# Kernel tuning notes

Measured on AMD Instinct MI355X. Metric: run time of the kernel, lower is better.

The kernel has to match this reference:

```python
import jax, jax.numpy as jnp
import numpy as np

B, S, D, H = 4, 2048, 1024, 16
HD = D // H  # head_dim = 64


def setup_inputs() -> dict:
    key = jax.random.key(0)
    ks = jax.random.split(key, 11)
    scale = 1.0 / np.sqrt(D)
    q = jax.random.normal(ks[0], (B, S, D), jnp.float32)
    k = jax.random.normal(ks[1], (B, S, D), jnp.float32)
    v = jax.random.normal(ks[2], (B, S, D), jnp.float32)
    # causal mask, broadcastable over [B, H, Sq, Sk]
    mask = jnp.tril(jnp.ones((S, S), bool))[None, None, :, :]
    Wq = jax.random.normal(ks[3], (D, D), jnp.float32) * scale
    bq = jnp.zeros((D,), jnp.float32)
    Wk = jax.random.normal(ks[4], (D, D), jnp.float32) * scale
    bk = jnp.zeros((D,), jnp.float32)
    Wv = jax.random.normal(ks[5], (D, D), jnp.float32) * scale
    bv = jnp.zeros((D,), jnp.float32)
    Wo = jax.random.normal(ks[6], (D, D), jnp.float32) * scale
    bo = jnp.zeros((D,), jnp.float32)
    return {"q": q, "k": k, "v": v, "mask": mask,
            "Wq": Wq, "bq": bq, "Wk": Wk, "bk": bk,
            "Wv": Wv, "bv": bv, "Wo": Wo, "bo": bo}


def reference(q, k, v, mask, Wq, bq, Wk, bk, Wv, bv, Wo, bo):
    b, sq, _ = q.shape
    sk = k.shape[1]
    # projections (torch Linear: x @ W.T + b)
    qh = (q @ Wq.T + bq).reshape(b, sq, H, HD)
    kh = (k @ Wk.T + bk).reshape(b, sk, H, HD)
    vh = (v @ Wv.T + bv).reshape(b, sk, H, HD)
    # scaled dot-product attention: [b, h, sq, sk]
    scores = jnp.einsum('bqhd,bkhd->bhqk', qh, kh) / jnp.sqrt(jnp.float32(HD))
    scores = jnp.where(mask, scores, jnp.float32(-jnp.inf))
    attn = jax.nn.softmax(scores, axis=-1)
    out = jnp.einsum('bhqk,bkhd->bqhd', attn, vh).reshape(b, sq, D)
    return out @ Wo.T + bo
```

## Files before the change

kernel.cpp:

```cpp
#include <hip/hip_runtime.h>
#include <hip/hip_bf16.h>
#include <cstdint>
#include <cstddef>

typedef __attribute__((ext_vector_type(4))) float f32x4;
typedef __attribute__((ext_vector_type(8))) __bf16 bf16x8;

constexpr int Bc = 4, Sc = 2048, Dc = 1024, Hc = 16, HDc = 64;
constexpr int Mrows = Bc * Sc;
constexpr int Kdim = Dc;

__device__ __forceinline__ void gload_lds16(const void* g, void* lds) {
  __builtin_amdgcn_global_load_lds(
      (const __attribute__((address_space(1))) void*)g,
      (__attribute__((address_space(3))) void*)lds, 16, 0, 0);
}

__global__ void cvt4_f32_to_bf16(const float* __restrict__ s0, const float* __restrict__ s1,
                                 const float* __restrict__ s2, const float* __restrict__ s3,
                                 __bf16* __restrict__ d0, __bf16* __restrict__ d1,
                                 __bf16* __restrict__ d2, __bf16* __restrict__ d3, int n4each) {
  int i = blockIdx.x * blockDim.x + threadIdx.x;
  int which = i / n4each, j = i - which * n4each;
  const float* s = which == 0 ? s0 : which == 1 ? s1 : which == 2 ? s2 : s3;
  __bf16* d = which == 0 ? d0 : which == 1 ? d1 : which == 2 ? d2 : d3;
  float4 f = ((const float4*)s)[j];
  union { __bf16 h[4]; uint2 u; } p;
  p.h[0] = (__bf16)f.x; p.h[1] = (__bf16)f.y;
  p.h[2] = (__bf16)f.z; p.h[3] = (__bf16)f.w;
  ((uint2*)d)[j] = p.u;
}

__global__ __launch_bounds__(256, 2)
void gemm_qkv(const float* __restrict__ qin, const float* __restrict__ kin,
              const float* __restrict__ vin, const __bf16* __restrict__ Wcat,
              const float* __restrict__ bq, const float* __restrict__ bk,
              const float* __restrict__ bv,
              __bf16* __restrict__ Qh, __bf16* __restrict__ Kh,
              __bf16* __restrict__ Vt, float qscale)
{
  __shared__ __align__(16) __bf16 As[128 * 32];
  __shared__ __align__(16) __bf16 Bs[128 * 32];
  const int tid = threadIdx.x;
  const int wave = tid >> 6, lane = tid & 63;
  const int wr = wave >> 1, wc = wave & 1;
  const int r = lane & 15, hi = lane >> 4;
  const int lin = (int)blockIdx.y * 24 + (int)blockIdx.x;
  const int xcd = lin & 7, s8 = lin >> 3;
  const int my = (xcd << 3) | (s8 / 24);
  const int mx = s8 % 24;
  const int m0 = my * 128, n0 = mx * 128;
  const int proj = n0 >> 10;
  const float* Xa = proj == 0 ? qin : proj == 1 ? kin : vin;

  f32x4 acc[4][4] = {};

  for (int k0 = 0; k0 < Kdim; k0 += 32) {
    #pragma unroll
    for (int c = 0; c < 2; ++c) {
      int chunk = c * 256 + tid;
      int row = chunk >> 2;
      int cw = chunk & 3;
      int hc = cw ^ (row & 3);
      const float* src = Xa + (size_t)(m0 + row) * Kdim + k0 + hc * 8;
      float4 f0 = *(const float4*)src;
      float4 f1 = *(const float4*)(src + 4);
      union { __bf16 h[8]; uint4 u; } pk;
      pk.h[0] = (__bf16)f0.x; pk.h[1] = (__bf16)f0.y;
      pk.h[2] = (__bf16)f0.z; pk.h[3] = (__bf16)f0.w;
      pk.h[4] = (__bf16)f1.x; pk.h[5] = (__bf16)f1.y;
      pk.h[6] = (__bf16)f1.z; pk.h[7] = (__bf16)f1.w;
      *(uint4*)&As[(size_t)chunk * 8] = pk.u;
    }
    #pragma unroll
    for (int c = 0; c < 2; ++c) {
      int chunk = c * 256 + wave * 64 + lane;
      int row = chunk >> 2;
      int hc = (chunk & 3) ^ (row & 3);
      gload_lds16(Wcat + (size_t)(n0 + row) * Kdim + k0 + hc * 8,
                  &Bs[(size_t)(c * 256 + wave * 64) * 8]);
    }
    __syncthreads();
    bf16x8 af[4], bfr[4];
    #pragma unroll
    for (int m = 0; m < 4; ++m) {
      int rowl = wr * 64 + m * 16 + r;
      af[m] = *(const bf16x8*)&As[rowl * 32 + ((hi ^ (rowl & 3)) * 8)];
    }
    #pragma unroll
    for (int n = 0; n < 4; ++n) {
      int rowl = wc * 64 + n * 16 + r;
      bfr[n] = *(const bf16x8*)&Bs[rowl * 32 + ((hi ^ (rowl & 3)) * 8)];
    }
    #pragma unroll
    for (int m = 0; m < 4; ++m)
      #pragma unroll
      for (int n = 0; n < 4; ++n)
        acc[m][n] = __builtin_amdgcn_mfma_f32_16x16x32_bf16(af[m], bfr[n], acc[m][n], 0, 0, 0);
    __syncthreads();
  }

  const float* bias = proj == 0 ? bq : proj == 1 ? bk : bv;
  if (proj < 2) {
    __bf16* out = proj == 0 ? Qh : Kh;
    const float sc = proj == 0 ? qscale : 1.0f;
    #pragma unroll
    for (int m = 0; m < 4; ++m)
      #pragma unroll
      for (int n = 0; n < 4; ++n)
        #pragma unroll
        for (int rg = 0; rg < 4; ++rg) {
          int row_g = m0 + wr * 64 + m * 16 + hi * 4 + rg;
          int col_g = n0 + wc * 64 + n * 16 + r;
          int c = col_g & 1023, h = c >> 6, d = c & 63;
          int b = row_g >> 11, s = row_g & (Sc - 1);
          float v = (acc[m][n][rg] + bias[c]) * sc;
          out[((((size_t)b * Hc + h) * Sc + s) << 6) + d] = (__bf16)v;
        }
  } else {
    #pragma unroll
    for (int m = 0; m < 4; ++m)
      #pragma unroll
      for (int n = 0; n < 4; ++n) {
        int row0 = m0 + wr * 64 + m * 16 + hi * 4;
        int col_g = n0 + wc * 64 + n * 16 + r;
        int c = col_g & 1023, h = c >> 6, d = c & 63;
        int b = row0 >> 11, s = row0 & (Sc - 1);
        union { __bf16 hh[4]; uint2 u; } w;
        #pragma unroll
        for (int rg = 0; rg < 4; ++rg)
          w.hh[rg] = (__bf16)(acc[m][n][rg] + bias[c]);
        *(uint2*)&Vt[((((size_t)b * Hc + h) * HDc + d) << 11) + s] = w.u;
      }
  }
}

__global__ __launch_bounds__(256, 2)
void gemm_out(const __bf16* __restrict__ A, const __bf16* __restrict__ Bw,
              const float* __restrict__ bias, float* __restrict__ outp)
{
  __shared__ __align__(16) __bf16 As[128 * 32];
  __shared__ __align__(16) __bf16 Bs[128 * 32];
  const int tid = threadIdx.x;
  const int wave = tid >> 6, lane = tid & 63;
  const int wr = wave >> 1, wc = wave & 1;
  const int r = lane & 15, hi = lane >> 4;
  const int lin = (int)blockIdx.y * 8 + (int)blockIdx.x;
  const int xcd = lin & 7, s8 = lin >> 3;
  const int m0 = (((xcd << 3) | (s8 >> 3)) ) * 128;
  const int n0 = (s8 & 7) * 128;

  f32x4 acc[4][4] = {};

  for (int k0 = 0; k0 < Kdim; k0 += 32) {
    #pragma unroll
    for (int c = 0; c < 2; ++c) {
      int chunk = c * 256 + wave * 64 + lane;
      int row = chunk >> 2;
      int hc = (chunk & 3) ^ (row & 3);
      gload_lds16(A  + (size_t)(m0 + row) * Kdim + k0 + hc * 8,
                  &As[(size_t)(c * 256 + wave * 64) * 8]);
      gload_lds16(Bw + (size_t)(n0 + row) * Kdim + k0 + hc * 8,
                  &Bs[(size_t)(c * 256 + wave * 64) * 8]);
    }
    __syncthreads();
    bf16x8 af[4], bfr[4];
    #pragma unroll
    for (int m = 0; m < 4; ++m) {
      int rowl = wr * 64 + m * 16 + r;
      af[m] = *(const bf16x8*)&As[rowl * 32 + ((hi ^ (rowl & 3)) * 8)];
    }
    #pragma unroll
    for (int n = 0; n < 4; ++n) {
      int rowl = wc * 64 + n * 16 + r;
      bfr[n] = *(const bf16x8*)&Bs[rowl * 32 + ((hi ^ (rowl & 3)) * 8)];
    }
    #pragma unroll
    for (int m = 0; m < 4; ++m)
      #pragma unroll
      for (int n = 0; n < 4; ++n)
        acc[m][n] = __builtin_amdgcn_mfma_f32_16x16x32_bf16(af[m], bfr[n], acc[m][n], 0, 0, 0);
    __syncthreads();
  }

  #pragma unroll
  for (int m = 0; m < 4; ++m)
    #pragma unroll
    for (int n = 0; n < 4; ++n)
      #pragma unroll
      for (int rg = 0; rg < 4; ++rg) {
        int row_g = m0 + wr * 64 + m * 16 + hi * 4 + rg;
        int col_g = n0 + wc * 64 + n * 16 + r;
        outp[(size_t)row_g * Dc + col_g] = acc[m][n][rg] + bias[col_g];
      }
}

__global__ __launch_bounds__(128, 2)
void attn_causal(const __bf16* __restrict__ Qh, const __bf16* __restrict__ Kh,
                 const __bf16* __restrict__ Vt, __bf16* __restrict__ outp)
{
  const int tid = threadIdx.x;
  const int wave = tid >> 6, lane = tid & 63;
  const int r = lane & 15, hi = lane >> 4;
  const int lin = (int)blockIdx.y * 32 + (int)blockIdx.x;
  const int xcd = lin & 7, s8 = lin >> 3;
  const int bh = (xcd << 3) | (s8 >> 5);
  const int px = s8 & 31;
  const int qh = wave ? (63 - px) : px;
  const int q0 = qh * 32;
  const __bf16* Q = Qh + (size_t)bh * (Sc * HDc);
  const __bf16* K = Kh + (size_t)bh * (Sc * HDc);
  const __bf16* V = Vt + (size_t)bh * (HDc * Sc);

  bf16x8 qf[2][2];
  #pragma unroll
  for (int m = 0; m < 2; ++m)
    #pragma unroll
    for (int kc = 0; kc < 2; ++kc)
      qf[m][kc] = *(const bf16x8*)&Q[(size_t)(q0 + m * 16 + r) * 64 + kc * 32 + hi * 8];

  f32x4 o_acc[2][4] = {};
  float mrow[2], lrow[2];
  #pragma unroll
  for (int m = 0; m < 2; ++m) { mrow[m] = -1e30f; lrow[m] = 0.f; }

  const int T = (qh >> 1) + 1;
  const int qloc_base = (qh & 1) * 32;

  bf16x8 kf[4][2], vf[4][2], pb[2][2];

  #pragma unroll
  for (int n = 0; n < 4; ++n)
    #pragma unroll
    for (int kc = 0; kc < 2; ++kc) {
      kf[n][kc] = *(const bf16x8*)&K[(size_t)(n * 16 + r) * 64 + kc * 32 + hi * 8];
      vf[n][kc] = *(const bf16x8*)&V[(size_t)(n * 16 + r) * Sc + kc * 32 + hi * 8];
    }

  for (int t = 0; t < T; ++t) {
    const bool diag = (t == T - 1);
    const int kvn = (t + 1) * 64;

    #pragma unroll
    for (int m = 0; m < 2; ++m) {
      f32x4 sn[4];
      __builtin_amdgcn_s_setprio(1);
      #pragma unroll
      for (int n = 0; n < 4; ++n) {
        f32x4 z = {0.f, 0.f, 0.f, 0.f};
        sn[n] = __builtin_amdgcn_mfma_f32_16x16x32_bf16(kf[n][0], qf[m][0], z, 0, 0, 0);
        sn[n] = __builtin_amdgcn_mfma_f32_16x16x32_bf16(kf[n][1], qf[m][1], sn[n], 0, 0, 0);
      }
      __builtin_amdgcn_s_setprio(0);
      if (diag) {
        #pragma unroll
        for (int n = 0; n < 4; ++n)
          #pragma unroll
          for (int rg = 0; rg < 4; ++rg)
            if (n * 16 + hi * 4 + rg > qloc_base + m * 16 + r) sn[n][rg] = -1e30f;
      }
      float mx = fmaxf(fmaxf(fmaxf(sn[0][0], sn[0][1]), fmaxf(sn[0][2], sn[0][3])),
                       fmaxf(fmaxf(sn[1][0], sn[1][1]), fmaxf(sn[1][2], sn[1][3])));
      mx = fmaxf(mx, fmaxf(fmaxf(fmaxf(sn[2][0], sn[2][1]), fmaxf(sn[2][2], sn[2][3])),
                           fmaxf(fmaxf(sn[3][0], sn[3][1]), fmaxf(sn[3][2], sn[3][3]))));
      mx = fmaxf(mx, __shfl_xor(mx, 16));
      mx = fmaxf(mx, __shfl_xor(mx, 32));
      float mloc = mrow[m];
      if (__any(mx > mloc + 8.f)) {
        float mnew = fmaxf(mloc, mx);
        float sc = __builtin_exp2f(mloc - mnew);
        lrow[m] *= sc;
        #pragma unroll
        for (int n = 0; n < 4; ++n) o_acc[m][n] *= sc;
        mrow[m] = mnew; mloc = mnew;
      }
      float rs = 0.f;
      #pragma unroll
      for (int n = 0; n < 4; ++n)
        #pragma unroll
        for (int rg = 0; rg < 4; ++rg) {
          float p = __builtin_exp2f(sn[n][rg] - mloc);
          sn[n][rg] = p;
          rs += p;
        }
      rs += __shfl_xor(rs, 16);
      rs += __shfl_xor(rs, 32);
      lrow[m] += rs;

      #pragma unroll
      for (int kc = 0; kc < 2; ++kc) {
        uint32_t p0a, p0b, p1a, p1b;
        asm("v_cvt_pk_bf16_f32 %0, %1, %2" : "=v"(p0a) : "v"(sn[2*kc][0]),   "v"(sn[2*kc][1]));
        asm("v_cvt_pk_bf16_f32 %0, %1, %2" : "=v"(p0b) : "v"(sn[2*kc][2]),   "v"(sn[2*kc][3]));
        asm("v_cvt_pk_bf16_f32 %0, %1, %2" : "=v"(p1a) : "v"(sn[2*kc+1][0]), "v"(sn[2*kc+1][1]));
        asm("v_cvt_pk_bf16_f32 %0, %1, %2" : "=v"(p1b) : "v"(sn[2*kc+1][2]), "v"(sn[2*kc+1][3]));
        asm("v_permlane32_swap_b32 %0, %1" : "+v"(p0a), "+v"(p1a));
        asm("v_permlane32_swap_b32 %0, %1" : "+v"(p0b), "+v"(p1b));
        uint32_t Xa = (uint32_t)__shfl_xor((int)p1a, 16);
        uint32_t Xb = (uint32_t)__shfl_xor((int)p1b, 16);
        uint32_t Ya = (uint32_t)__shfl_xor((int)p0a, 16);
        uint32_t Yb = (uint32_t)__shfl_xor((int)p0b, 16);
        union { uint32_t u[4]; bf16x8 v; } pk;
        pk.u[0] = (hi & 1) ? Xa : p0a;
        pk.u[1] = (hi & 1) ? Xb : p0b;
        pk.u[2] = (hi & 1) ? p1a : Ya;
        pk.u[3] = (hi & 1) ? p1b : Yb;
        pb[m][kc] = pk.v;
      }
    }

    if (t + 1 < T) {
      #pragma unroll
      for (int n = 0; n < 4; ++n)
        #pragma unroll
        for (int kc = 0; kc < 2; ++kc)
          kf[n][kc] = *(const bf16x8*)&K[(size_t)(kvn + n * 16 + r) * 64 + kc * 32 + hi * 8];
    }

    __builtin_amdgcn_s_setprio(1);
    #pragma unroll
    for (int m = 0; m < 2; ++m)
      #pragma unroll
      for (int n = 0; n < 4; ++n) {
        o_acc[m][n] = __builtin_amdgcn_mfma_f32_16x16x32_bf16(vf[n][0], pb[m][0], o_acc[m][n], 0, 0, 0);
        o_acc[m][n] = __builtin_amdgcn_mfma_f32_16x16x32_bf16(vf[n][1], pb[m][1], o_acc[m][n], 0, 0, 0);
      }
    __builtin_amdgcn_s_setprio(0);

    if (t + 1 < T) {
      #pragma unroll
      for (int n = 0; n < 4; ++n)
        #pragma unroll
        for (int kc = 0; kc < 2; ++kc)
          vf[n][kc] = *(const bf16x8*)&V[(size_t)(n * 16 + r) * Sc + kvn + kc * 32 + hi * 8];
    }
  }

  const int b = bh >> 4, h = bh & 15;
  #pragma unroll
  for (int m = 0; m < 2; ++m) {
    float inv = 1.f / lrow[m];
    size_t row = (size_t)b * Sc + q0 + m * 16 + r;
    #pragma unroll
    for (int n = 0; n < 4; ++n) {
      union { __bf16 hh[4]; uint2 u; } w;
      #pragma unroll
      for (int rg = 0; rg < 4; ++rg)
        w.hh[rg] = (__bf16)(o_acc[m][n][rg] * inv);
      int col = h * 64 + n * 16 + hi * 4;
      *(uint2*)&outp[row * Dc + col] = w.u;
    }
  }
}

extern "C" void kernel_launch(void* const* d_in, const int* in_sizes, int n_in,
                              void* d_out, int out_size, void* d_ws, size_t ws_size,
                              hipStream_t stream) {
  const float* q  = (const float*)d_in[0];
  const float* k  = (const float*)d_in[1];
  const float* v  = (const float*)d_in[2];
  const float* Wq = (const float*)d_in[4];
  const float* bq = (const float*)d_in[5];
  const float* Wk = (const float*)d_in[6];
  const float* bk = (const float*)d_in[7];
  const float* Wv = (const float*)d_in[8];
  const float* bv = (const float*)d_in[9];
  const float* Wo = (const float*)d_in[10];
  const float* bo = (const float*)d_in[11];

  char* ws = (char*)d_ws;
  constexpr size_t MB = 1u << 20;
  __bf16* Wcat = (__bf16*)(ws + 0 * MB);
  __bf16* Wkb  = (__bf16*)(ws + 2 * MB);
  __bf16* Wvb  = (__bf16*)(ws + 4 * MB);
  __bf16* Wob  = (__bf16*)(ws + 6 * MB);
  __bf16* Xbf  = (__bf16*)(ws + 8 * MB);
  __bf16* QhB  = (__bf16*)(ws + 24 * MB);
  __bf16* KhB  = (__bf16*)(ws + 40 * MB);
  __bf16* VtB  = (__bf16*)(ws + 56 * MB);

  const int nW4 = (Dc * Dc) / 4;
  cvt4_f32_to_bf16<<<(4 * nW4) / 256, 256, 0, stream>>>(Wq, Wk, Wv, Wo, Wcat, Wkb, Wvb, Wob, nW4);

  const float qscale = 0.125f * 1.44269504f;
  gemm_qkv<<<dim3(24, Mrows / 128), 256, 0, stream>>>(q, k, v, Wcat, bq, bk, bv,
                                                      QhB, KhB, VtB, qscale);

  attn_causal<<<dim3(32, Bc * Hc), 128, 0, stream>>>(QhB, KhB, VtB, Xbf);

  gemm_out<<<dim3(8, Mrows / 128), 256, 0, stream>>>(Xbf, Wob, bo, (float*)d_out);
}
```

Baseline: 267.1 us.

## Switch attention kernel to 32x32x16 MFMA with 32-key tiles

The causal attention kernel moves from 16x16x32 MFMA to 32x32x16 MFMA. Each wave now covers 32 query rows with one score tile per 32-key step instead of two 16-row slices per 64-key step. This simplifies the softmax reductions and the P-fragment repacking, removing the shfl_xor(16) exchanges so only permlane32 swaps remain. In exchange there are twice as many loop iterations, each with a smaller KV tile. That gives less latency hiding per iteration for the register-prefetched K and V loads, and a different register footprint.

```diff
diff --git a/kernel.cpp b/kernel.cpp
--- a/kernel.cpp
+++ b/kernel.cpp
@@ -4,6 +4,7 @@
 #include <cstddef>
 
 typedef __attribute__((ext_vector_type(4))) float f32x4;
+typedef __attribute__((ext_vector_type(16))) float f32x16;
 typedef __attribute__((ext_vector_type(8))) __bf16 bf16x8;
 
 constexpr int Bc = 4, Sc = 2048, Dc = 1024, Hc = 16, HDc = 64;
@@ -201,7 +202,8 @@
 {
   const int tid = threadIdx.x;
   const int wave = tid >> 6, lane = tid & 63;
-  const int r = lane & 15, hi = lane >> 4;
+  const int c32 = lane & 31;
+  const int h5 = lane >> 5;
   const int lin = (int)blockIdx.y * 32 + (int)blockIdx.x;
   const int xcd = lin & 7, s8 = lin >> 3;
   const int bh = (xcd << 3) | (s8 >> 5);
@@ -212,144 +214,122 @@
   const __bf16* K = Kh + (size_t)bh * (Sc * HDc);
   const __bf16* V = Vt + (size_t)bh * (HDc * Sc);
 
-  bf16x8 qf[2][2];
-  #pragma unroll
-  for (int m = 0; m < 2; ++m)
-    #pragma unroll
-    for (int kc = 0; kc < 2; ++kc)
-      qf[m][kc] = *(const bf16x8*)&Q[(size_t)(q0 + m * 16 + r) * 64 + kc * 32 + hi * 8];
-
-  f32x4 o_acc[2][4] = {};
-  float mrow[2], lrow[2];
-  #pragma unroll
-  for (int m = 0; m < 2; ++m) { mrow[m] = -1e30f; lrow[m] = 0.f; }
-
-  const int T = (qh >> 1) + 1;
-  const int qloc_base = (qh & 1) * 32;
-
-  bf16x8 kf[4][2], vf[4][2], pb[2][2];
-
-  #pragma unroll
-  for (int n = 0; n < 4; ++n)
-    #pragma unroll
-    for (int kc = 0; kc < 2; ++kc) {
-      kf[n][kc] = *(const bf16x8*)&K[(size_t)(n * 16 + r) * 64 + kc * 32 + hi * 8];
-      vf[n][kc] = *(const bf16x8*)&V[(size_t)(n * 16 + r) * Sc + kc * 32 + hi * 8];
-    }
+  bf16x8 qf[4];
+  #pragma unroll
+  for (int dc = 0; dc < 4; ++dc)
+    qf[dc] = *(const bf16x8*)&Q[(size_t)(q0 + c32) * 64 + dc * 16 + h5 * 8];
+
+  f32x16 o0 = {}, o1 = {};
+  float mrow = -1e30f, lrow = 0.f;
+
+  const int T = qh + 1;
+  bf16x8 kf[4], vf0[2], vf1[2];
+
+  #pragma unroll
+  for (int dc = 0; dc < 4; ++dc)
+    kf[dc] = *(const bf16x8*)&K[(size_t)c32 * 64 + dc * 16 + h5 * 8];
+  #pragma unroll
+  for (int kc = 0; kc < 2; ++kc) {
+    vf0[kc] = *(const bf16x8*)&V[(size_t)c32 * Sc + kc * 16 + h5 * 8];
+    vf1[kc] = *(const bf16x8*)&V[(size_t)(32 + c32) * Sc + kc * 16 + h5 * 8];
+  }
 
   for (int t = 0; t < T; ++t) {
     const bool diag = (t == T - 1);
-    const int kvn = (t + 1) * 64;
-
-    #pragma unroll
-    for (int m = 0; m < 2; ++m) {
-      f32x4 sn[4];
-      __builtin_amdgcn_s_setprio(1);
-      #pragma unroll
-      for (int n = 0; n < 4; ++n) {
-        f32x4 z = {0.f, 0.f, 0.f, 0.f};
-        sn[n] = __builtin_amdgcn_mfma_f32_16x16x32_bf16(kf[n][0], qf[m][0], z, 0, 0, 0);
-        sn[n] = __builtin_amdgcn_mfma_f32_16x16x32_bf16(kf[n][1], qf[m][1], sn[n], 0, 0, 0);
+    const int kvn = (t + 1) * 32;
+
+    f32x16 sn = {};
+    __builtin_amdgcn_s_setprio(1);
+    sn = __builtin_amdgcn_mfma_f32_32x32x16_bf16(kf[0], qf[0], sn, 0, 0, 0);
+    sn = __builtin_amdgcn_mfma_f32_32x32x16_bf16(kf[1], qf[1], sn, 0, 0, 0);
+    sn = __builtin_amdgcn_mfma_f32_32x32x16_bf16(kf[2], qf[2], sn, 0, 0, 0);
+    sn = __builtin_amdgcn_mfma_f32_32x32x16_bf16(kf[3], qf[3], sn, 0, 0, 0);
+    __builtin_amdgcn_s_setprio(0);
+
+    if (diag) {
+      #pragma unroll
+      for (int reg = 0; reg < 16; ++reg)
+        if ((reg & 3) + 8 * (reg >> 2) + 4 * h5 > c32) sn[reg] = -1e30f;
+    }
+
+    float mx = fmaxf(fmaxf(fmaxf(sn[0], sn[1]), fmaxf(sn[2], sn[3])),
+                     fmaxf(fmaxf(sn[4], sn[5]), fmaxf(sn[6], sn[7])));
+    mx = fmaxf(mx, fmaxf(fmaxf(fmaxf(sn[8], sn[9]), fmaxf(sn[10], sn[11])),
+                         fmaxf(fmaxf(sn[12], sn[13]), fmaxf(sn[14], sn[15]))));
+    mx = fmaxf(mx, __shfl_xor(mx, 32));
+    if (__any(mx > mrow + 8.f)) {
+      float mnew = fmaxf(mrow, mx);
+      float sc = __builtin_exp2f(mrow - mnew);
+      lrow *= sc;
+      o0 *= sc;
+      o1 *= sc;
+      mrow = mnew;
+    }
+    float rs = 0.f;
+    #pragma unroll
+    for (int reg = 0; reg < 16; ++reg) {
+      float p = __builtin_exp2f(sn[reg] - mrow);
+      sn[reg] = p;
+      rs += p;
+    }
+    rs += __shfl_xor(rs, 32);
+    lrow += rs;
+
+    uint32_t u0, u1, u2, u3, u4, u5, u6, u7;
+    asm("v_cvt_pk_bf16_f32 %0, %1, %2" : "=v"(u0) : "v"(sn[0]),  "v"(sn[1]));
+    asm("v_cvt_pk_bf16_f32 %0, %1, %2" : "=v"(u1) : "v"(sn[2]),  "v"(sn[3]));
+    asm("v_cvt_pk_bf16_f32 %0, %1, %2" : "=v"(u2) : "v"(sn[4]),  "v"(sn[5]));
+    asm("v_cvt_pk_bf16_f32 %0, %1, %2" : "=v"(u3) : "v"(sn[6]),  "v"(sn[7]));
+    asm("v_cvt_pk_bf16_f32 %0, %1, %2" : "=v"(u4) : "v"(sn[8]),  "v"(sn[9]));
+    asm("v_cvt_pk_bf16_f32 %0, %1, %2" : "=v"(u5) : "v"(sn[10]), "v"(sn[11]));
+    asm("v_cvt_pk_bf16_f32 %0, %1, %2" : "=v"(u6) : "v"(sn[12]), "v"(sn[13]));
+    asm("v_cvt_pk_bf16_f32 %0, %1, %2" : "=v"(u7) : "v"(sn[14]), "v"(sn[15]));
+    asm("v_permlane32_swap_b32 %0, %1" : "+v"(u0), "+v"(u2));
+    asm("v_permlane32_swap_b32 %0, %1" : "+v"(u1), "+v"(u3));
+    asm("v_permlane32_swap_b32 %0, %1" : "+v"(u4), "+v"(u6));
+    asm("v_permlane32_swap_b32 %0, %1" : "+v"(u5), "+v"(u7));
+    union { uint32_t w[4]; bf16x8 v; } pb0, pb1;
+    pb0.w[0] = u0; pb0.w[1] = u1; pb0.w[2] = u2; pb0.w[3] = u3;
+    pb1.w[0] = u4; pb1.w[1] = u5; pb1.w[2] = u6; pb1.w[3] = u7;
+
+    if (t + 1 < T) {
+      #pragma unroll
+      for (int dc = 0; dc < 4; ++dc)
+        kf[dc] = *(const bf16x8*)&K[(size_t)(kvn + c32) * 64 + dc * 16 + h5 * 8];
+    }
+
+    __builtin_amdgcn_s_setprio(1);
+    o0 = __builtin_amdgcn_mfma_f32_32x32x16_bf16(vf0[0], pb0.v, o0, 0, 0, 0);
+    o0 = __builtin_amdgcn_mfma_f32_32x32x16_bf16(vf0[1], pb1.v, o0, 0, 0, 0);
+    o1 = __builtin_amdgcn_mfma_f32_32x32x16_bf16(vf1[0], pb0.v, o1, 0, 0, 0);
+    o1 = __builtin_amdgcn_mfma_f32_32x32x16_bf16(vf1[1], pb1.v, o1, 0, 0, 0);
+    __builtin_amdgcn_s_setprio(0);
+
+    if (t + 1 < T) {
+      #pragma unroll
+      for (int kc = 0; kc < 2; ++kc) {
+        vf0[kc] = *(const bf16x8*)&V[(size_t)c32 * Sc + kvn + kc * 16 + h5 * 8];
+        vf1[kc] = *(const bf16x8*)&V[(size_t)(32 + c32) * Sc + kvn + kc * 16 + h5 * 8];
       }
-      __builtin_amdgcn_s_setprio(0);
-      if (diag) {
-        #pragma unroll
-        for (int n = 0; n < 4; ++n)
-          #pragma unroll
-          for (int rg = 0; rg < 4; ++rg)
-            if (n * 16 + hi * 4 + rg > qloc_base + m * 16 + r) sn[n][rg] = -1e30f;
-      }
-      float mx = fmaxf(fmaxf(fmaxf(sn[0][0], sn[0][1]), fmaxf(sn[0][2], sn[0][3])),
-                       fmaxf(fmaxf(sn[1][0], sn[1][1]), fmaxf(sn[1][2], sn[1][3])));
-      mx = fmaxf(mx, fmaxf(fmaxf(fmaxf(sn[2][0], sn[2][1]), fmaxf(sn[2][2], sn[2][3])),
-                           fmaxf(fmaxf(sn[3][0], sn[3][1]), fmaxf(sn[3][2], sn[3][3]))));
-      mx = fmaxf(mx, __shfl_xor(mx, 16));
-      mx = fmaxf(mx, __shfl_xor(mx, 32));
-      float mloc = mrow[m];
-      if (__any(mx > mloc + 8.f)) {
-        float mnew = fmaxf(mloc, mx);
-        float sc = __builtin_exp2f(mloc - mnew);
-        lrow[m] *= sc;
-        #pragma unroll
-        for (int n = 0; n < 4; ++n) o_acc[m][n] *= sc;
-        mrow[m] = mnew; mloc = mnew;
-      }
-      float rs = 0.f;
-      #pragma unroll
-      for (int n = 0; n < 4; ++n)
-        #pragma unroll
-        for (int rg = 0; rg < 4; ++rg) {
-          float p = __builtin_exp2f(sn[n][rg] - mloc);
-          sn[n][rg] = p;
-          rs += p;
-        }
-      rs += __shfl_xor(rs, 16);
-      rs += __shfl_xor(rs, 32);
-      lrow[m] += rs;
-
-      #pragma unroll
-      for (int kc = 0; kc < 2; ++kc) {
-        uint32_t p0a, p0b, p1a, p1b;
-        asm("v_cvt_pk_bf16_f32 %0, %1, %2" : "=v"(p0a) : "v"(sn[2*kc][0]),   "v"(sn[2*kc][1]));
-        asm("v_cvt_pk_bf16_f32 %0, %1, %2" : "=v"(p0b) : "v"(sn[2*kc][2]),   "v"(sn[2*kc][3]));
-        asm("v_cvt_pk_bf16_f32 %0, %1, %2" : "=v"(p1a) : "v"(sn[2*kc+1][0]), "v"(sn[2*kc+1][1]));
-        asm("v_cvt_pk_bf16_f32 %0, %1, %2" : "=v"(p1b) : "v"(sn[2*kc+1][2]), "v"(sn[2*kc+1][3]));
-        asm("v_permlane32_swap_b32 %0, %1" : "+v"(p0a), "+v"(p1a));
-        asm("v_permlane32_swap_b32 %0, %1" : "+v"(p0b), "+v"(p1b));
-        uint32_t Xa = (uint32_t)__shfl_xor((int)p1a, 16);
-        uint32_t Xb = (uint32_t)__shfl_xor((int)p1b, 16);
-        uint32_t Ya = (uint32_t)__shfl_xor((int)p0a, 16);
-        uint32_t Yb = (uint32_t)__shfl_xor((int)p0b, 16);
-        union { uint32_t u[4]; bf16x8 v; } pk;
-        pk.u[0] = (hi & 1) ? Xa : p0a;
-        pk.u[1] = (hi & 1) ? Xb : p0b;
-        pk.u[2] = (hi & 1) ? p1a : Ya;
-        pk.u[3] = (hi & 1) ? p1b : Yb;
-        pb[m][kc] = pk.v;
-      }
-    }
-
-    if (t + 1 < T) {
-      #pragma unroll
-      for (int n = 0; n < 4; ++n)
-        #pragma unroll
-        for (int kc = 0; kc < 2; ++kc)
-          kf[n][kc] = *(const bf16x8*)&K[(size_t)(kvn + n * 16 + r) * 64 + kc * 32 + hi * 8];
-    }
-
-    __builtin_amdgcn_s_setprio(1);
-    #pragma unroll
-    for (int m = 0; m < 2; ++m)
-      #pragma unroll
-      for (int n = 0; n < 4; ++n) {
-        o_acc[m][n] = __builtin_amdgcn_mfma_f32_16x16x32_bf16(vf[n][0], pb[m][0], o_acc[m][n], 0, 0, 0);
-        o_acc[m][n] = __builtin_amdgcn_mfma_f32_16x16x32_bf16(vf[n][1], pb[m][1], o_acc[m][n], 0, 0, 0);
-      }
-    __builtin_amdgcn_s_setprio(0);
-
-    if (t + 1 < T) {
-      #pragma unroll
-      for (int n = 0; n < 4; ++n)
-        #pragma unroll
-        for (int kc = 0; kc < 2; ++kc)
-          vf[n][kc] = *(const bf16x8*)&V[(size_t)(n * 16 + r) * Sc + kvn + kc * 32 + hi * 8];
     }
   }
 
   const int b = bh >> 4, h = bh & 15;
-  #pragma unroll
-  for (int m = 0; m < 2; ++m) {
-    float inv = 1.f / lrow[m];
-    size_t row = (size_t)b * Sc + q0 + m * 16 + r;
-    #pragma unroll
-    for (int n = 0; n < 4; ++n) {
-      union { __bf16 hh[4]; uint2 u; } w;
-      #pragma unroll
-      for (int rg = 0; rg < 4; ++rg)
-        w.hh[rg] = (__bf16)(o_acc[m][n][rg] * inv);
-      int col = h * 64 + n * 16 + hi * 4;
-      *(uint2*)&outp[row * Dc + col] = w.u;
-    }
+  const float inv = 1.f / lrow;
+  __bf16* obase = outp + ((size_t)b * Sc + q0 + c32) * Dc + h * 64;
+  #pragma unroll
+  for (int rq = 0; rq < 4; ++rq) {
+    union { __bf16 hh[4]; uint2 u; } w;
+    #pragma unroll
+    for (int rr = 0; rr < 4; ++rr) w.hh[rr] = (__bf16)(o0[rq * 4 + rr] * inv);
+    *(uint2*)&obase[rq * 8 + h5 * 4] = w.u;
+  }
+  #pragma unroll
+  for (int rq = 0; rq < 4; ++rq) {
+    union { __bf16 hh[4]; uint2 u; } w;
+    #pragma unroll
+    for (int rr = 0; rr < 4; ++rr) w.hh[rr] = (__bf16)(o1[rq * 4 + rr] * inv);
+    *(uint2*)&obase[32 + rq * 8 + h5 * 4] = w.u;
   }
 }
 
```

New measurement: 238.4 us, median of 2. -10.7%, faster.
